# Performance work log

Measured on AMD Instinct MI355X. Metric: run time of the kernel, lower is better.

Reference implementation:

```python
import jax, jax.numpy as jnp
import numpy as np


def setup_inputs() -> dict:
    key = jax.random.key(0)
    k1, k2 = jax.random.split(key)
    B, S, D = 64, 1024, 768
    batch = jax.random.normal(k1, (B, S, D), dtype=jnp.float32)
    # nn.init.uniform_(proj, -0.05, 0.05)
    proj = jax.random.uniform(k2, (D, D), minval=-0.05, maxval=0.05, dtype=jnp.float32)
    return {"batch": batch, "proj": proj}


def reference(batch, proj):
    """dists[b,i,j] = (h_i - h_j)^T A (h_i - h_j)
    Expanded: h_i^T A h_i + h_j^T A h_j - h_i^T A h_j - h_j^T A h_i.
    Avoids the O(B*S^2*D) diffs tensor of the original.
    """
    # P[b,i,:] = h_i^T A  -> (B, S, D)
    P = jnp.einsum('bid,de->bie', batch, proj)
    # cross[b,i,j] = h_i^T A h_j -> (B, S, S)
    cross = jnp.einsum('bie,bje->bij', P, batch)
    q = jnp.einsum('bii->bi', cross)  # h_i^T A h_i, (B, S)
    dists = q[:, :, None] + q[:, None, :] - cross - jnp.swapaxes(cross, 1, 2)
    return dists
```

## Files before the change

kernel.cpp:

```cpp
#include <hip/hip_runtime.h>

#define GLOBAL_AS __attribute__((address_space(1)))
#define LDS_AS    __attribute__((address_space(3)))

typedef __bf16 bf16_t;
typedef __bf16 bf16x8 __attribute__((ext_vector_type(8)));
typedef __bf16 bf16x4 __attribute__((ext_vector_type(4)));
typedef float  f32x4  __attribute__((ext_vector_type(4)));

#define BATCH 64
#define SEQ   1024
#define DIM   768
#define BS_ROWS (BATCH * SEQ)

__device__ __forceinline__ void gl2lds16(const void* g, void* l) {
    __builtin_amdgcn_global_load_lds((GLOBAL_AS const void*)g, (LDS_AS void*)l, 16, 0, 0);
}

__global__ void k_convert(const float* __restrict__ x, bf16_t* __restrict__ y, int n8) {
    int gid = blockIdx.x * 256 + threadIdx.x;
    if (gid >= n8) return;
    const float4* xp = (const float4*)x;
    float4 a = xp[gid * 2];
    float4 b = xp[gid * 2 + 1];
    bf16x8 v;
    v[0] = (bf16_t)a.x; v[1] = (bf16_t)a.y; v[2] = (bf16_t)a.z; v[3] = (bf16_t)a.w;
    v[4] = (bf16_t)b.x; v[5] = (bf16_t)b.y; v[6] = (bf16_t)b.z; v[7] = (bf16_t)b.w;
    ((bf16x8*)y)[gid] = v;
}

__global__ void k_asym(const float* __restrict__ A, bf16_t* __restrict__ S_, int n) {
    int idx = blockIdx.x * 256 + threadIdx.x;
    if (idx >= n) return;
    int d = idx / DIM;
    int e = idx - d * DIM;
    S_[idx] = (bf16_t)(A[idx] + A[e * DIM + d]);
}


__global__ void k_gemm1(const bf16_t* __restrict__ H, const bf16_t* __restrict__ Ag,
                        bf16_t* __restrict__ M) {
    __shared__ bf16_t Asm[128 * 32];
    __shared__ bf16_t Bsm[128 * 32];
    const int t = threadIdx.x;
    const int row0 = blockIdx.y * 128;
    const int col0 = blockIdx.x * 128;
    const int ln = t & 63, w = t >> 6;
    const int wr = w >> 1, wc = w & 1;
    const int r = ln & 15, qd = ln >> 4;
    const int sseg = qd ^ ((r >> 1) & 3);

    const int srow = t >> 2;
    const int gseg = (t & 3) ^ ((t >> 3) & 3);
    const bf16_t* gA0 = H  + (size_t)(row0 + srow) * DIM + gseg * 8;
    const bf16_t* gA1 = gA0 + (size_t)64 * DIM;
    const bf16_t* gB0 = Ag + (size_t)(col0 + srow) * DIM + gseg * 8;
    const bf16_t* gB1 = gB0 + (size_t)64 * DIM;

    f32x4 acc[4][4] = {};

    for (int k0 = 0; k0 < DIM; k0 += 32) {
        gl2lds16(gA0 + k0, &Asm[t * 8]);
        gl2lds16(gA1 + k0, &Asm[2048 + t * 8]);
        gl2lds16(gB0 + k0, &Bsm[t * 8]);
        gl2lds16(gB1 + k0, &Bsm[2048 + t * 8]);
        __syncthreads();

        bf16x8 af[4], bf[4];
#pragma unroll
        for (int mt = 0; mt < 4; ++mt) {
            int m = wr * 64 + mt * 16 + r;
            af[mt] = *(const bf16x8*)&Asm[m * 32 + sseg * 8];
        }
#pragma unroll
        for (int nt = 0; nt < 4; ++nt) {
            int n = wc * 64 + nt * 16 + r;
            bf[nt] = *(const bf16x8*)&Bsm[n * 32 + sseg * 8];
        }
#pragma unroll
        for (int mt = 0; mt < 4; ++mt)
#pragma unroll
            for (int nt = 0; nt < 4; ++nt)
                acc[mt][nt] = __builtin_amdgcn_mfma_f32_16x16x32_bf16(
                    af[mt], bf[nt], acc[mt][nt], 0, 0, 0);
        __syncthreads();
    }

#pragma unroll
    for (int mt = 0; mt < 4; ++mt) {
#pragma unroll
        for (int rI = 0; rI < 4; ++rI) {
            int row = row0 + wr * 64 + mt * 16 + qd * 4 + rI;
            size_t base = (size_t)row * DIM + col0 + wc * 64;
#pragma unroll
            for (int nt = 0; nt < 4; ++nt)
                M[base + nt * 16 + r] = (bf16_t)acc[mt][nt][rI];
        }
    }
}

__global__ void k_q(const bf16_t* __restrict__ M, const bf16_t* __restrict__ H,
                    float* __restrict__ qv) {
    int t = threadIdx.x;
    int w = t >> 6, ln = t & 63;
    int row = blockIdx.x * 4 + w;
    const bf16_t* mp = M + (size_t)row * DIM;
    const bf16_t* hp = H + (size_t)row * DIM;
    float acc = 0.f;
#pragma unroll
    for (int j = 0; j < 3; ++j) {
        int e = j * 256 + ln * 4;
        bf16x4 mv = *(const bf16x4*)&mp[e];
        bf16x4 hv = *(const bf16x4*)&hp[e];
#pragma unroll
        for (int u = 0; u < 4; ++u) acc += (float)mv[u] * (float)hv[u];
    }
#pragma unroll
    for (int off = 32; off > 0; off >>= 1) acc += __shfl_down(acc, off, 64);
    if (ln == 0) qv[row] = 0.5f * acc;
}

__global__ void k_gemm2(const bf16_t* __restrict__ M, const bf16_t* __restrict__ H,
                        const float* __restrict__ qv, float* __restrict__ out) {
    __shared__ bf16_t Asm[128 * 32];
    __shared__ bf16_t Bsm[128 * 32];
    const int t = threadIdx.x;
    const int b = blockIdx.z;
    const int row0 = blockIdx.y * 128;
    const int col0 = blockIdx.x * 128;
    const int ln = t & 63, w = t >> 6;
    const int wr = w >> 1, wc = w & 1;
    const int r = ln & 15, qd = ln >> 4;
    const int sseg = qd ^ ((r >> 1) & 3);

    const bf16_t* Mb = M + (size_t)b * SEQ * DIM;
    const bf16_t* Hb = H + (size_t)b * SEQ * DIM;

    const int srow = t >> 2;
    const int gseg = (t & 3) ^ ((t >> 3) & 3);
    const bf16_t* gA0 = Mb + (size_t)(row0 + srow) * DIM + gseg * 8;
    const bf16_t* gA1 = gA0 + (size_t)64 * DIM;
    const bf16_t* gB0 = Hb + (size_t)(col0 + srow) * DIM + gseg * 8;
    const bf16_t* gB1 = gB0 + (size_t)64 * DIM;

    f32x4 acc[4][4] = {};

    for (int k0 = 0; k0 < DIM; k0 += 32) {
        gl2lds16(gA0 + k0, &Asm[t * 8]);
        gl2lds16(gA1 + k0, &Asm[2048 + t * 8]);
        gl2lds16(gB0 + k0, &Bsm[t * 8]);
        gl2lds16(gB1 + k0, &Bsm[2048 + t * 8]);
        __syncthreads();

        bf16x8 af[4], bf[4];
#pragma unroll
        for (int mt = 0; mt < 4; ++mt) {
            int m = wr * 64 + mt * 16 + r;
            af[mt] = *(const bf16x8*)&Asm[m * 32 + sseg * 8];
        }
#pragma unroll
        for (int nt = 0; nt < 4; ++nt) {
            int n = wc * 64 + nt * 16 + r;
            bf[nt] = *(const bf16x8*)&Bsm[n * 32 + sseg * 8];
        }
#pragma unroll
        for (int mt = 0; mt < 4; ++mt)
#pragma unroll
            for (int nt = 0; nt < 4; ++nt)
                acc[mt][nt] = __builtin_amdgcn_mfma_f32_16x16x32_bf16(
                    af[mt], bf[nt], acc[mt][nt], 0, 0, 0);
        __syncthreads();
    }

    const float* qb = qv + b * SEQ;
    float qc[4];
#pragma unroll
    for (int nt = 0; nt < 4; ++nt) qc[nt] = qb[col0 + wc * 64 + nt * 16 + r];

#pragma unroll
    for (int mt = 0; mt < 4; ++mt) {
#pragma unroll
        for (int rI = 0; rI < 4; ++rI) {
            int row = row0 + wr * 64 + mt * 16 + qd * 4 + rI;
            float qr = qb[row];
            size_t base = ((size_t)b * SEQ + row) * SEQ + col0 + wc * 64;
#pragma unroll
            for (int nt = 0; nt < 4; ++nt)
                out[base + nt * 16 + r] = qr + qc[nt] - acc[mt][nt][rI];
        }
    }
}

extern "C" void kernel_launch(void* const* d_in, const int* in_sizes, int n_in,
                              void* d_out, int out_size, void* d_ws, size_t ws_size,
                              hipStream_t stream) {
    const float* batch = (const float*)d_in[0];
    const float* proj  = (const float*)d_in[1];
    float* out = (float*)d_out;

    char* ws = (char*)d_ws;
    bf16_t* Hb = (bf16_t*)ws;
    bf16_t* Mb = (bf16_t*)(ws + 100663296);
    bf16_t* Ab = (bf16_t*)(ws + 201326592);
    float*  qv = (float*)(ws + 202506240);

    k_convert<<<24576, 256, 0, stream>>>(batch, Hb, 6291456);
    k_asym<<<2304, 256, 0, stream>>>(proj, Ab, DIM * DIM);
    k_gemm1<<<dim3(DIM / 128, BS_ROWS / 128), 256, 0, stream>>>(Hb, Ab, Mb);
    k_q<<<BS_ROWS / 4, 256, 0, stream>>>(Mb, Hb, qv);
    k_gemm2<<<dim3(SEQ / 128, SEQ / 128, BATCH), 256, 0, stream>>>(Mb, Hb, qv, out);
}
```

Baseline: 699.7 us.

## Exploit output symmetry in gemm2, fuse q reduction into gemm1 epilogue

The second GEMM now computes only upper-triangular tile pairs (36 of 64 per batch). For each off-diagonal tile it also writes the transposed copy through an LDS staging buffer, which roughly halves the MFMA work and operand reads. The q diagonal term is folded into the gemm1 epilogue using wave shuffles and atomicAdd, which removes the separate k_q pass but needs a zeroing kernel first. Both GEMMs get XCD-aware block remapping. The cost is extra LDS transpose traffic, extra syncs, and atomics.

```diff
diff --git a/kernel.cpp b/kernel.cpp
--- a/kernel.cpp
+++ b/kernel.cpp
@@ -15,6 +15,11 @@
 
 __device__ __forceinline__ void gl2lds16(const void* g, void* l) {
     __builtin_amdgcn_global_load_lds((GLOBAL_AS const void*)g, (LDS_AS void*)l, 16, 0, 0);
+}
+
+__global__ void k_zero(float* __restrict__ p, int n) {
+    int gid = blockIdx.x * 256 + threadIdx.x;
+    if (gid < n) p[gid] = 0.f;
 }
 
 __global__ void k_convert(const float* __restrict__ x, bf16_t* __restrict__ y, int n8) {
@@ -37,14 +42,15 @@
     S_[idx] = (bf16_t)(A[idx] + A[e * DIM + d]);
 }
 
-
 __global__ void k_gemm1(const bf16_t* __restrict__ H, const bf16_t* __restrict__ Ag,
-                        bf16_t* __restrict__ M) {
+                        bf16_t* __restrict__ M, float* __restrict__ qv) {
     __shared__ bf16_t Asm[128 * 32];
     __shared__ bf16_t Bsm[128 * 32];
     const int t = threadIdx.x;
-    const int row0 = blockIdx.y * 128;
-    const int col0 = blockIdx.x * 128;
+    const int g = blockIdx.x;
+    const int tile = (g & 7) * 384 + (g >> 3);
+    const int row0 = (tile / 6) * 128;
+    const int col0 = (tile % 6) * 128;
     const int ln = t & 63, w = t >> 6;
     const int wr = w >> 1, wc = w & 1;
     const int r = ln & 15, qd = ln >> 4;
@@ -92,42 +98,40 @@
         for (int rI = 0; rI < 4; ++rI) {
             int row = row0 + wr * 64 + mt * 16 + qd * 4 + rI;
             size_t base = (size_t)row * DIM + col0 + wc * 64;
-#pragma unroll
-            for (int nt = 0; nt < 4; ++nt)
-                M[base + nt * 16 + r] = (bf16_t)acc[mt][nt][rI];
-        }
-    }
-}
-
-__global__ void k_q(const bf16_t* __restrict__ M, const bf16_t* __restrict__ H,
-                    float* __restrict__ qv) {
-    int t = threadIdx.x;
-    int w = t >> 6, ln = t & 63;
-    int row = blockIdx.x * 4 + w;
-    const bf16_t* mp = M + (size_t)row * DIM;
-    const bf16_t* hp = H + (size_t)row * DIM;
-    float acc = 0.f;
-#pragma unroll
-    for (int j = 0; j < 3; ++j) {
-        int e = j * 256 + ln * 4;
-        bf16x4 mv = *(const bf16x4*)&mp[e];
-        bf16x4 hv = *(const bf16x4*)&hp[e];
-#pragma unroll
-        for (int u = 0; u < 4; ++u) acc += (float)mv[u] * (float)hv[u];
-    }
-#pragma unroll
-    for (int off = 32; off > 0; off >>= 1) acc += __shfl_down(acc, off, 64);
-    if (ln == 0) qv[row] = 0.5f * acc;
+            float s = 0.f;
+#pragma unroll
+            for (int nt = 0; nt < 4; ++nt) {
+                bf16_t mv = (bf16_t)acc[mt][nt][rI];
+                M[base + nt * 16 + r] = mv;
+                s += (float)mv * (float)H[base + nt * 16 + r];
+            }
+            s += __shfl_xor(s, 1, 64);
+            s += __shfl_xor(s, 2, 64);
+            s += __shfl_xor(s, 4, 64);
+            s += __shfl_xor(s, 8, 64);
+            if (r == 0) atomicAdd(&qv[row], 0.5f * s);
+        }
+    }
 }
 
 __global__ void k_gemm2(const bf16_t* __restrict__ M, const bf16_t* __restrict__ H,
                         const float* __restrict__ qv, float* __restrict__ out) {
-    __shared__ bf16_t Asm[128 * 32];
-    __shared__ bf16_t Bsm[128 * 32];
+    __shared__ __align__(16) char smem[16640];
+    bf16_t* Asm = (bf16_t*)smem;
+    bf16_t* Bsm = (bf16_t*)(smem + 8192);
+    float*  Tsm = (float*)smem;
+
     const int t = threadIdx.x;
-    const int b = blockIdx.z;
-    const int row0 = blockIdx.y * 128;
-    const int col0 = blockIdx.x * 128;
+    const int g = blockIdx.x;
+    const int u = (g & 7) * 288 + (g >> 3);
+    const int b = u / 36;
+    int l = u - b * 36;
+    int ti = 0;
+    while (l >= 8 - ti) { l -= 8 - ti; ++ti; }
+    const int tj = ti + l;
+    const int row0 = ti * 128;
+    const int col0 = tj * 128;
+
     const int ln = t & 63, w = t >> 6;
     const int wr = w >> 1, wc = w & 1;
     const int r = ln & 15, qd = ln >> 4;
@@ -189,6 +193,41 @@
                 out[base + nt * 16 + r] = qr + qc[nt] - acc[mt][nt][rI];
         }
     }
+
+    if (ti != tj) {
+#pragma unroll
+        for (int c = 0; c < 4; ++c) {
+            __syncthreads();
+            if (wr == (c >> 1)) {
+                const int m0 = (c & 1) * 2;
+#pragma unroll
+                for (int mi = 0; mi < 2; ++mi) {
+                    const int mt = m0 + mi;
+#pragma unroll
+                    for (int rI = 0; rI < 4; ++rI) {
+                        int lrow = mi * 16 + qd * 4 + rI;
+                        int row = row0 + wr * 64 + mt * 16 + qd * 4 + rI;
+                        float qr = qb[row];
+#pragma unroll
+                        for (int nt = 0; nt < 4; ++nt) {
+                            int lcol = wc * 64 + nt * 16 + r;
+                            Tsm[lrow * 130 + lcol] = qr + qc[nt] - acc[mt][nt][rI];
+                        }
+                    }
+                }
+            }
+            __syncthreads();
+            const int rowbase = row0 + 32 * c;
+#pragma unroll
+            for (int i = 0; i < 16; ++i) {
+                int lin = i * 256 + t;
+                int lrow = lin & 31;
+                int lcol = lin >> 5;
+                out[((size_t)b * SEQ + col0 + lcol) * SEQ + rowbase + lrow] =
+                    Tsm[lrow * 130 + lcol];
+            }
+        }
+    }
 }
 
 extern "C" void kernel_launch(void* const* d_in, const int* in_sizes, int n_in,
@@ -204,9 +243,9 @@
     bf16_t* Ab = (bf16_t*)(ws + 201326592);
     float*  qv = (float*)(ws + 202506240);
 
+    k_zero<<<256, 256, 0, stream>>>(qv, BS_ROWS);
     k_convert<<<24576, 256, 0, stream>>>(batch, Hb, 6291456);
     k_asym<<<2304, 256, 0, stream>>>(proj, Ab, DIM * DIM);
-    k_gemm1<<<dim3(DIM / 128, BS_ROWS / 128), 256, 0, stream>>>(Hb, Ab, Mb);
-    k_q<<<BS_ROWS / 4, 256, 0, stream>>>(Mb, Hb, qv);
-    k_gemm2<<<dim3(SEQ / 128, SEQ / 128, BATCH), 256, 0, stream>>>(Mb, Hb, qv, out);
-}
+    k_gemm1<<<3072, 256, 0, stream>>>(Hb, Ab, Mb, qv);
+    k_gemm2<<<2304, 256, 0, stream>>>(Mb, Hb, qv, out);
+}
```

Result: no change. 687.7 us (-1.7%).
